# Kernel optimization log

Hardware: AMD Instinct MI355X
Metric: run time of the kernel (lower is better)

Reference implementation:

```python
import jax, jax.numpy as jnp
import numpy as np

N_NODES = 100_000
N_EDGES = 1_600_000
D_IN = 128
D_OUT = 128


def setup_inputs() -> dict:
    key = jax.random.key(0)
    k1, k2, k3, k4, k5 = jax.random.split(key, 5)
    feature = jax.random.normal(k1, (N_NODES, D_IN), dtype=jnp.float32)
    W = jax.random.normal(k2, (D_IN, D_OUT), dtype=jnp.float32) * 0.05
    b = jax.random.normal(k3, (D_OUT,), dtype=jnp.float32) * 0.05
    src = jax.random.randint(k4, (N_EDGES,), 0, N_NODES, dtype=jnp.int32)
    dst = jax.random.randint(k5, (N_EDGES,), 0, N_NODES, dtype=jnp.int32)
    return {"feature": feature, "W": W, "b": b, "src": src, "dst": dst}


def reference(feature, W, b, src, dst):
    N = feature.shape[0]
    # in-degrees (number of incoming edges per node)
    in_deg = jax.ops.segment_sum(
        jnp.ones(dst.shape[0], dtype=feature.dtype), dst, num_segments=N
    )  # [N]
    # degree-constraint scaling: h = x / sqrt(in_deg + 1)
    feat = feature * (1.0 / jnp.sqrt(in_deg + 1.0))[:, None]  # [N, D]
    # copy_u messages + mean reduce over incoming edges
    msg = feat[src]  # [E, D]
    summed = jax.ops.segment_sum(msg, dst, num_segments=N)  # [N, D]
    cnt = in_deg[:, None]
    h = jnp.where(cnt > 0, summed / jnp.maximum(cnt, 1.0), 0.0)  # DGL mean -> 0 for isolated nodes
    # apply_mod linear
    return h @ W + b
```

## Files before the change

### kernel.cpp

```cpp
#include <hip/hip_runtime.h>
#include <math.h>


#define D 128
#define MT 32
#define CAP 48
#define CPAD 16

typedef short short8 __attribute__((ext_vector_type(8)));
typedef float f32x4 __attribute__((ext_vector_type(4)));

__device__ inline unsigned short f2b(float f) {
    unsigned u = __float_as_uint(f);
    return (unsigned short)((u + 0x7FFFu + ((u >> 16) & 1u)) >> 16);
}
#define B2F(u) __uint_as_float(((unsigned)(u)) << 16)

__global__ __launch_bounds__(256) void k_fill(const int* __restrict__ src,
                                              const int* __restrict__ dst,
                                              int* __restrict__ cnt_p,
                                              int* __restrict__ ell,
                                              int ne, int nn) {
    int i = blockIdx.x * 256 + threadIdx.x;
    int e0 = i * 4;
    if (e0 + 4 <= ne) {
        int4 sv = ((const int4*)src)[i];
        int4 dv = ((const int4*)dst)[i];
        int p0 = atomicAdd(&cnt_p[dv.x * CPAD], 1); if (p0 < CAP) ell[(size_t)dv.x * CAP + p0] = sv.x;
        int p1 = atomicAdd(&cnt_p[dv.y * CPAD], 1); if (p1 < CAP) ell[(size_t)dv.y * CAP + p1] = sv.y;
        int p2 = atomicAdd(&cnt_p[dv.z * CPAD], 1); if (p2 < CAP) ell[(size_t)dv.z * CAP + p2] = sv.z;
        int p3 = atomicAdd(&cnt_p[dv.w * CPAD], 1); if (p3 < CAP) ell[(size_t)dv.w * CAP + p3] = sv.w;
    } else {
        for (int e = e0; e < ne; ++e) {
            int d = dst[e];
            int p = atomicAdd(&cnt_p[d * CPAD], 1);
            if (p < CAP) ell[(size_t)d * CAP + p] = src[e];
        }
    }
}

__global__ __launch_bounds__(256) void k_mid(const int* __restrict__ cnt_p,
                                             const float* __restrict__ W,
                                             int* __restrict__ cnt_c,
                                             float* __restrict__ scale,
                                             unsigned short* __restrict__ Wt,
                                             int nn, int sb) {
    int t = threadIdx.x;
    if (blockIdx.x < sb) {
        int n = blockIdx.x * 256 + t;
        if (n < nn) {
            int c = cnt_p[n * CPAD];
            cnt_c[n] = c;
            scale[n] = rsqrtf((float)c + 1.0f);
        }
        return;
    }
    int d = t & 127, k0 = (t >> 7) * 64;
    for (int k = 0; k < 64; ++k)
        Wt[d * D + k0 + k] = f2b(W[(size_t)(k0 + k) * D + d]);
}

__global__ __launch_bounds__(256) void k_gemm(const float* __restrict__ feature,
                                              const unsigned short* __restrict__ Wt,
                                              unsigned short* __restrict__ Yb,
                                              int nn) {
    int t = threadIdx.x;
    int w = t >> 6, l = t & 63;
    int rg = w & 1, ch = w >> 1;
    int base = blockIdx.x * MT;
    int r = base + rg * 16 + (l & 15);
    if (r >= nn) r = nn - 1;
    int kl = (l >> 4) * 8;

    short8 af[4];
    const float* fr = feature + (size_t)r * D;
#pragma unroll
    for (int kc = 0; kc < 4; ++kc) {
        float4 x = *(const float4*)(fr + kc * 32 + kl);
        float4 y = *(const float4*)(fr + kc * 32 + kl + 4);
        short8 a;
        a[0] = (short)f2b(x.x); a[1] = (short)f2b(x.y);
        a[2] = (short)f2b(x.z); a[3] = (short)f2b(x.w);
        a[4] = (short)f2b(y.x); a[5] = (short)f2b(y.y);
        a[6] = (short)f2b(y.z); a[7] = (short)f2b(y.w);
        af[kc] = a;
    }

    f32x4 acc[4];
#pragma unroll
    for (int ct = 0; ct < 4; ++ct) acc[ct] = (f32x4){0.f, 0.f, 0.f, 0.f};

#pragma unroll
    for (int ct = 0; ct < 4; ++ct) {
        int c = ch * 64 + ct * 16 + (l & 15);
        const unsigned short* wr = Wt + (size_t)c * D;
#pragma unroll
        for (int kc = 0; kc < 4; ++kc) {
            short8 b = *(const short8*)(wr + kc * 32 + kl);
            acc[ct] = __builtin_amdgcn_mfma_f32_16x16x32_bf16(af[kc], b, acc[ct], 0, 0, 0);
        }
    }

#pragma unroll
    for (int ct = 0; ct < 4; ++ct) {
        int c = ch * 64 + ct * 16 + (l & 15);
        int r0 = base + rg * 16 + (l >> 4) * 4;
#pragma unroll
        for (int j = 0; j < 4; ++j) {
            int row = r0 + j;
            if (row < nn) Yb[(size_t)row * D + c] = f2b(acc[ct][j]);
        }
    }
}

__global__ __launch_bounds__(256) void k_agg(const unsigned short* __restrict__ Yb,
                                             const float* __restrict__ bias,
                                             const int* __restrict__ cnt,
                                             const float* __restrict__ scale,
                                             const int* __restrict__ ell,
                                             float* __restrict__ out,
                                             int n_nodes) {
    int t = threadIdx.x;
    int wave = t >> 6, lane = t & 63;
    int hw = lane >> 5, sl = lane & 31;
    int base = blockIdx.x * MT;

    const ushort4* y4 = (const ushort4*)Yb;
    float4 bv = ((const float4*)bias)[sl];

#pragma unroll
    for (int j = 0; j < 4; ++j) {
        int n = base + wave * 8 + j * 2 + hw;
        bool valid = (n < n_nodes);
        int c = valid ? cnt[n] : 0;
        if (c > CAP) c = CAP;
        float4 a0 = make_float4(0.f, 0.f, 0.f, 0.f), a1 = a0, a2 = a0, a3 = a0;
        if (c > 0) {
            int slot = sl < c ? sl : c - 1;
            int v = ell[(size_t)n * CAP + slot];
            int iv0 = ((unsigned)v < (unsigned)n_nodes) ? v : 0;
            float sv0 = scale[iv0];
            int eb = 0;
            while (eb < c) {
                int nv = c - eb; if (nv > 32) nv = 32;
                int e = 0;
                for (; e + 8 <= nv; e += 8) {
                    int i0 = __shfl(iv0, e + 0, 32), i1 = __shfl(iv0, e + 1, 32);
                    int i2 = __shfl(iv0, e + 2, 32), i3 = __shfl(iv0, e + 3, 32);
                    int i4 = __shfl(iv0, e + 4, 32), i5 = __shfl(iv0, e + 5, 32);
                    int i6 = __shfl(iv0, e + 6, 32), i7 = __shfl(iv0, e + 7, 32);
                    float c0 = __shfl(sv0, e + 0, 32), c1 = __shfl(sv0, e + 1, 32);
                    float c2 = __shfl(sv0, e + 2, 32), c3 = __shfl(sv0, e + 3, 32);
                    float c4 = __shfl(sv0, e + 4, 32), c5 = __shfl(sv0, e + 5, 32);
                    float c6 = __shfl(sv0, e + 6, 32), c7 = __shfl(sv0, e + 7, 32);
                    ushort4 u0 = y4[(size_t)i0 * 32 + sl], u1 = y4[(size_t)i1 * 32 + sl];
                    ushort4 u2 = y4[(size_t)i2 * 32 + sl], u3 = y4[(size_t)i3 * 32 + sl];
                    ushort4 u4 = y4[(size_t)i4 * 32 + sl], u5 = y4[(size_t)i5 * 32 + sl];
                    ushort4 u6 = y4[(size_t)i6 * 32 + sl], u7 = y4[(size_t)i7 * 32 + sl];
                    a0.x = fmaf(B2F(u0.x), c0, a0.x); a0.y = fmaf(B2F(u0.y), c0, a0.y);
                    a0.z = fmaf(B2F(u0.z), c0, a0.z); a0.w = fmaf(B2F(u0.w), c0, a0.w);
                    a1.x = fmaf(B2F(u1.x), c1, a1.x); a1.y = fmaf(B2F(u1.y), c1, a1.y);
                    a1.z = fmaf(B2F(u1.z), c1, a1.z); a1.w = fmaf(B2F(u1.w), c1, a1.w);
                    a2.x = fmaf(B2F(u2.x), c2, a2.x); a2.y = fmaf(B2F(u2.y), c2, a2.y);
                    a2.z = fmaf(B2F(u2.z), c2, a2.z); a2.w = fmaf(B2F(u2.w), c2, a2.w);
                    a3.x = fmaf(B2F(u3.x), c3, a3.x); a3.y = fmaf(B2F(u3.y), c3, a3.y);
                    a3.z = fmaf(B2F(u3.z), c3, a3.z); a3.w = fmaf(B2F(u3.w), c3, a3.w);
                    a0.x = fmaf(B2F(u4.x), c4, a0.x); a0.y = fmaf(B2F(u4.y), c4, a0.y);
                    a0.z = fmaf(B2F(u4.z), c4, a0.z); a0.w = fmaf(B2F(u4.w), c4, a0.w);
                    a1.x = fmaf(B2F(u5.x), c5, a1.x); a1.y = fmaf(B2F(u5.y), c5, a1.y);
                    a1.z = fmaf(B2F(u5.z), c5, a1.z); a1.w = fmaf(B2F(u5.w), c5, a1.w);
                    a2.x = fmaf(B2F(u6.x), c6, a2.x); a2.y = fmaf(B2F(u6.y), c6, a2.y);
                    a2.z = fmaf(B2F(u6.z), c6, a2.z); a2.w = fmaf(B2F(u6.w), c6, a2.w);
                    a3.x = fmaf(B2F(u7.x), c7, a3.x); a3.y = fmaf(B2F(u7.y), c7, a3.y);
                    a3.z = fmaf(B2F(u7.z), c7, a3.z); a3.w = fmaf(B2F(u7.w), c7, a3.w);
                }
                for (; e + 4 <= nv; e += 4) {
                    int i0 = __shfl(iv0, e + 0, 32), i1 = __shfl(iv0, e + 1, 32);
                    int i2 = __shfl(iv0, e + 2, 32), i3 = __shfl(iv0, e + 3, 32);
                    float c0 = __shfl(sv0, e + 0, 32), c1 = __shfl(sv0, e + 1, 32);
                    float c2 = __shfl(sv0, e + 2, 32), c3 = __shfl(sv0, e + 3, 32);
                    ushort4 u0 = y4[(size_t)i0 * 32 + sl], u1 = y4[(size_t)i1 * 32 + sl];
                    ushort4 u2 = y4[(size_t)i2 * 32 + sl], u3 = y4[(size_t)i3 * 32 + sl];
                    a0.x = fmaf(B2F(u0.x), c0, a0.x); a0.y = fmaf(B2F(u0.y), c0, a0.y);
                    a0.z = fmaf(B2F(u0.z), c0, a0.z); a0.w = fmaf(B2F(u0.w), c0, a0.w);
                    a1.x = fmaf(B2F(u1.x), c1, a1.x); a1.y = fmaf(B2F(u1.y), c1, a1.y);
                    a1.z = fmaf(B2F(u1.z), c1, a1.z); a1.w = fmaf(B2F(u1.w), c1, a1.w);
                    a2.x = fmaf(B2F(u2.x), c2, a2.x); a2.y = fmaf(B2F(u2.y), c2, a2.y);
                    a2.z = fmaf(B2F(u2.z), c2, a2.z); a2.w = fmaf(B2F(u2.w), c2, a2.w);
                    a3.x = fmaf(B2F(u3.x), c3, a3.x); a3.y = fmaf(B2F(u3.y), c3, a3.y);
                    a3.z = fmaf(B2F(u3.z), c3, a3.z); a3.w = fmaf(B2F(u3.w), c3, a3.w);
                }
                for (; e < nv; ++e) {
                    int s = __shfl(iv0, e, 32);
                    float cc = __shfl(sv0, e, 32);
                    ushort4 u = y4[(size_t)s * 32 + sl];
                    a0.x = fmaf(B2F(u.x), cc, a0.x); a0.y = fmaf(B2F(u.y), cc, a0.y);
                    a0.z = fmaf(B2F(u.z), cc, a0.z); a0.w = fmaf(B2F(u.w), cc, a0.w);
                }
                eb += 32;
                if (eb < c) {
                    int rem = c - eb;
                    int slot2 = eb + (sl < rem ? sl : rem - 1);
                    if (slot2 > CAP - 1) slot2 = CAP - 1;
                    int v2 = ell[(size_t)n * CAP + slot2];
                    iv0 = ((unsigned)v2 < (unsigned)n_nodes) ? v2 : 0;
                    sv0 = scale[iv0];
                }
            }
        }
        if (valid) {
            float invn = (c > 0) ? (1.0f / (float)c) : 0.f;
            float4 r;
            r.x = (a0.x + a1.x + a2.x + a3.x) * invn + bv.x;
            r.y = (a0.y + a1.y + a2.y + a3.y) * invn + bv.y;
            r.z = (a0.z + a1.z + a2.z + a3.z) * invn + bv.z;
            r.w = (a0.w + a1.w + a2.w + a3.w) * invn + bv.w;
            ((float4*)out)[(size_t)n * 32 + sl] = r;
        }
    }
}

extern "C" void kernel_launch(void* const* d_in, const int* in_sizes, int n_in,
                              void* d_out, int out_size, void* d_ws, size_t ws_size,
                              hipStream_t stream) {
    const float* feature = (const float*)d_in[0];
    const float* W = (const float*)d_in[1];
    const float* bias = (const float*)d_in[2];
    const int* src = (const int*)d_in[3];
    const int* dst = (const int*)d_in[4];
    float* out = (float*)d_out;

    int n_nodes = in_sizes[0] / D;
    int n_edges = in_sizes[3];
    (void)n_in; (void)out_size; (void)ws_size;

    char* ws = (char*)d_ws;
    size_t o = 0;
    auto alloc = [&](size_t bytes) { void* p = ws + o; o += (bytes + 511) & ~(size_t)511; return p; };
    int* cnt_p = (int*)alloc((size_t)n_nodes * CPAD * 4);
    int* ell = (int*)alloc((size_t)n_nodes * CAP * 4);
    unsigned short* Yb = (unsigned short*)alloc((size_t)n_nodes * D * 2);
    int* cnt_c = (int*)alloc((size_t)n_nodes * 4);
    float* scale = (float*)alloc((size_t)n_nodes * 4);
    unsigned short* Wt = (unsigned short*)alloc((size_t)D * D * 2);

    hipMemsetAsync(cnt_p, 0, (size_t)n_nodes * CPAD * 4, stream);

    int fb = (n_edges + 1023) / 1024;
    int sb = (n_nodes + 255) / 256;
    int tiles = (n_nodes + MT - 1) / MT;

    k_fill<<<fb, 256, 0, stream>>>(src, dst, cnt_p, ell, n_edges, n_nodes);
    k_mid<<<sb + 1, 256, 0, stream>>>(cnt_p, W, cnt_c, scale, Wt, n_nodes, sb);
    k_gemm<<<tiles, 256, 0, stream>>>(feature, Wt, Yb, n_nodes);
    k_agg<<<tiles, 256, 0, stream>>>(Yb, bias, cnt_c, scale, ell, out, n_nodes);
}
```

Before: 339.6 us.

## Store first neighbor indices inline in padded count line with spill array

Uses the otherwise padded 64-byte counter line per node to hold the count plus the first 15 source indices. Extra neighbors go to a separate spill array. The aggregation kernel loads count and up to 31 indices in one pass (16 lanes from the count line, 16 from spill), which removes the separate count array and the dependent count-then-index load chain. Edges past 31 are handled by a scalar per-lane loop, and the inline stores put edge writes on the same cache line as the atomic counter, which may add contention.

```diff
diff --git a/kernel.cpp b/kernel.cpp
--- a/kernel.cpp
+++ b/kernel.cpp
@@ -4,8 +4,10 @@
 
 #define D 128
 #define MT 32
-#define CAP 48
 #define CPAD 16
+#define INL 15
+#define CAPT 48
+#define SCAP 33
 
 typedef short short8 __attribute__((ext_vector_type(8)));
 typedef float f32x4 __attribute__((ext_vector_type(4)));
@@ -18,41 +20,36 @@
 
 __global__ __launch_bounds__(256) void k_fill(const int* __restrict__ src,
                                               const int* __restrict__ dst,
-                                              int* __restrict__ cnt_p,
-                                              int* __restrict__ ell,
+                                              int* __restrict__ cl,
+                                              int* __restrict__ spill,
                                               int ne, int nn) {
+#define PUT(s_, d_) { int p = atomicAdd(&cl[(d_) * CPAD], 1);                  \
+        if (p < INL) cl[(d_) * CPAD + 1 + p] = (s_);                           \
+        else if (p < CAPT) spill[(size_t)(d_) * SCAP + (p - INL)] = (s_); }
     int i = blockIdx.x * 256 + threadIdx.x;
     int e0 = i * 4;
     if (e0 + 4 <= ne) {
         int4 sv = ((const int4*)src)[i];
         int4 dv = ((const int4*)dst)[i];
-        int p0 = atomicAdd(&cnt_p[dv.x * CPAD], 1); if (p0 < CAP) ell[(size_t)dv.x * CAP + p0] = sv.x;
-        int p1 = atomicAdd(&cnt_p[dv.y * CPAD], 1); if (p1 < CAP) ell[(size_t)dv.y * CAP + p1] = sv.y;
-        int p2 = atomicAdd(&cnt_p[dv.z * CPAD], 1); if (p2 < CAP) ell[(size_t)dv.z * CAP + p2] = sv.z;
-        int p3 = atomicAdd(&cnt_p[dv.w * CPAD], 1); if (p3 < CAP) ell[(size_t)dv.w * CAP + p3] = sv.w;
+        PUT(sv.x, dv.x)
+        PUT(sv.y, dv.y)
+        PUT(sv.z, dv.z)
+        PUT(sv.w, dv.w)
     } else {
-        for (int e = e0; e < ne; ++e) {
-            int d = dst[e];
-            int p = atomicAdd(&cnt_p[d * CPAD], 1);
-            if (p < CAP) ell[(size_t)d * CAP + p] = src[e];
-        }
-    }
-}
-
-__global__ __launch_bounds__(256) void k_mid(const int* __restrict__ cnt_p,
+        for (int e = e0; e < ne; ++e) PUT(src[e], dst[e])
+    }
+#undef PUT
+}
+
+__global__ __launch_bounds__(256) void k_mid(const int* __restrict__ cl,
                                              const float* __restrict__ W,
-                                             int* __restrict__ cnt_c,
                                              float* __restrict__ scale,
                                              unsigned short* __restrict__ Wt,
                                              int nn, int sb) {
     int t = threadIdx.x;
     if (blockIdx.x < sb) {
         int n = blockIdx.x * 256 + t;
-        if (n < nn) {
-            int c = cnt_p[n * CPAD];
-            cnt_c[n] = c;
-            scale[n] = rsqrtf((float)c + 1.0f);
-        }
+        if (n < nn) scale[n] = rsqrtf((float)cl[n * CPAD] + 1.0f);
         return;
     }
     int d = t & 127, k0 = (t >> 7) * 64;
@@ -115,9 +112,9 @@
 
 __global__ __launch_bounds__(256) void k_agg(const unsigned short* __restrict__ Yb,
                                              const float* __restrict__ bias,
-                                             const int* __restrict__ cnt,
+                                             const int* __restrict__ cl,
+                                             const int* __restrict__ spill,
                                              const float* __restrict__ scale,
-                                             const int* __restrict__ ell,
                                              float* __restrict__ out,
                                              int n_nodes) {
     int t = threadIdx.x;
@@ -132,80 +129,79 @@
     for (int j = 0; j < 4; ++j) {
         int n = base + wave * 8 + j * 2 + hw;
         bool valid = (n < n_nodes);
-        int c = valid ? cnt[n] : 0;
-        if (c > CAP) c = CAP;
+        int nc = valid ? n : 0;
+        int lv;
+        if (sl < 16) lv = cl[nc * CPAD + sl];
+        else         lv = spill[(size_t)nc * SCAP + (sl - 16)];
+        int c = __shfl(lv, 0, 32);
+        if (!valid) c = 0;
+        if (c > CAPT) c = CAPT;
         float4 a0 = make_float4(0.f, 0.f, 0.f, 0.f), a1 = a0, a2 = a0, a3 = a0;
         if (c > 0) {
-            int slot = sl < c ? sl : c - 1;
-            int v = ell[(size_t)n * CAP + slot];
-            int iv0 = ((unsigned)v < (unsigned)n_nodes) ? v : 0;
+            int iv0 = ((unsigned)lv < (unsigned)n_nodes) ? lv : 0;
             float sv0 = scale[iv0];
-            int eb = 0;
-            while (eb < c) {
-                int nv = c - eb; if (nv > 32) nv = 32;
-                int e = 0;
-                for (; e + 8 <= nv; e += 8) {
-                    int i0 = __shfl(iv0, e + 0, 32), i1 = __shfl(iv0, e + 1, 32);
-                    int i2 = __shfl(iv0, e + 2, 32), i3 = __shfl(iv0, e + 3, 32);
-                    int i4 = __shfl(iv0, e + 4, 32), i5 = __shfl(iv0, e + 5, 32);
-                    int i6 = __shfl(iv0, e + 6, 32), i7 = __shfl(iv0, e + 7, 32);
-                    float c0 = __shfl(sv0, e + 0, 32), c1 = __shfl(sv0, e + 1, 32);
-                    float c2 = __shfl(sv0, e + 2, 32), c3 = __shfl(sv0, e + 3, 32);
-                    float c4 = __shfl(sv0, e + 4, 32), c5 = __shfl(sv0, e + 5, 32);
-                    float c6 = __shfl(sv0, e + 6, 32), c7 = __shfl(sv0, e + 7, 32);
-                    ushort4 u0 = y4[(size_t)i0 * 32 + sl], u1 = y4[(size_t)i1 * 32 + sl];
-                    ushort4 u2 = y4[(size_t)i2 * 32 + sl], u3 = y4[(size_t)i3 * 32 + sl];
-                    ushort4 u4 = y4[(size_t)i4 * 32 + sl], u5 = y4[(size_t)i5 * 32 + sl];
-                    ushort4 u6 = y4[(size_t)i6 * 32 + sl], u7 = y4[(size_t)i7 * 32 + sl];
-                    a0.x = fmaf(B2F(u0.x), c0, a0.x); a0.y = fmaf(B2F(u0.y), c0, a0.y);
-                    a0.z = fmaf(B2F(u0.z), c0, a0.z); a0.w = fmaf(B2F(u0.w), c0, a0.w);
-                    a1.x = fmaf(B2F(u1.x), c1, a1.x); a1.y = fmaf(B2F(u1.y), c1, a1.y);
-                    a1.z = fmaf(B2F(u1.z), c1, a1.z); a1.w = fmaf(B2F(u1.w), c1, a1.w);
-                    a2.x = fmaf(B2F(u2.x), c2, a2.x); a2.y = fmaf(B2F(u2.y), c2, a2.y);
-                    a2.z = fmaf(B2F(u2.z), c2, a2.z); a2.w = fmaf(B2F(u2.w), c2, a2.w);
-                    a3.x = fmaf(B2F(u3.x), c3, a3.x); a3.y = fmaf(B2F(u3.y), c3, a3.y);
-                    a3.z = fmaf(B2F(u3.z), c3, a3.z); a3.w = fmaf(B2F(u3.w), c3, a3.w);
-                    a0.x = fmaf(B2F(u4.x), c4, a0.x); a0.y = fmaf(B2F(u4.y), c4, a0.y);
-                    a0.z = fmaf(B2F(u4.z), c4, a0.z); a0.w = fmaf(B2F(u4.w), c4, a0.w);
-                    a1.x = fmaf(B2F(u5.x), c5, a1.x); a1.y = fmaf(B2F(u5.y), c5, a1.y);
-                    a1.z = fmaf(B2F(u5.z), c5, a1.z); a1.w = fmaf(B2F(u5.w), c5, a1.w);
-                    a2.x = fmaf(B2F(u6.x), c6, a2.x); a2.y = fmaf(B2F(u6.y), c6, a2.y);
-                    a2.z = fmaf(B2F(u6.z), c6, a2.z); a2.w = fmaf(B2F(u6.w), c6, a2.w);
-                    a3.x = fmaf(B2F(u7.x), c7, a3.x); a3.y = fmaf(B2F(u7.y), c7, a3.y);
-                    a3.z = fmaf(B2F(u7.z), c7, a3.z); a3.w = fmaf(B2F(u7.w), c7, a3.w);
-                }
-                for (; e + 4 <= nv; e += 4) {
-                    int i0 = __shfl(iv0, e + 0, 32), i1 = __shfl(iv0, e + 1, 32);
-                    int i2 = __shfl(iv0, e + 2, 32), i3 = __shfl(iv0, e + 3, 32);
-                    float c0 = __shfl(sv0, e + 0, 32), c1 = __shfl(sv0, e + 1, 32);
-                    float c2 = __shfl(sv0, e + 2, 32), c3 = __shfl(sv0, e + 3, 32);
-                    ushort4 u0 = y4[(size_t)i0 * 32 + sl], u1 = y4[(size_t)i1 * 32 + sl];
-                    ushort4 u2 = y4[(size_t)i2 * 32 + sl], u3 = y4[(size_t)i3 * 32 + sl];
-                    a0.x = fmaf(B2F(u0.x), c0, a0.x); a0.y = fmaf(B2F(u0.y), c0, a0.y);
-                    a0.z = fmaf(B2F(u0.z), c0, a0.z); a0.w = fmaf(B2F(u0.w), c0, a0.w);
-                    a1.x = fmaf(B2F(u1.x), c1, a1.x); a1.y = fmaf(B2F(u1.y), c1, a1.y);
-                    a1.z = fmaf(B2F(u1.z), c1, a1.z); a1.w = fmaf(B2F(u1.w), c1, a1.w);
-                    a2.x = fmaf(B2F(u2.x), c2, a2.x); a2.y = fmaf(B2F(u2.y), c2, a2.y);
-                    a2.z = fmaf(B2F(u2.z), c2, a2.z); a2.w = fmaf(B2F(u2.w), c2, a2.w);
-                    a3.x = fmaf(B2F(u3.x), c3, a3.x); a3.y = fmaf(B2F(u3.y), c3, a3.y);
-                    a3.z = fmaf(B2F(u3.z), c3, a3.z); a3.w = fmaf(B2F(u3.w), c3, a3.w);
-                }
-                for (; e < nv; ++e) {
-                    int s = __shfl(iv0, e, 32);
-                    float cc = __shfl(sv0, e, 32);
-                    ushort4 u = y4[(size_t)s * 32 + sl];
-                    a0.x = fmaf(B2F(u.x), cc, a0.x); a0.y = fmaf(B2F(u.y), cc, a0.y);
-                    a0.z = fmaf(B2F(u.z), cc, a0.z); a0.w = fmaf(B2F(u.w), cc, a0.w);
-                }
-                eb += 32;
-                if (eb < c) {
-                    int rem = c - eb;
-                    int slot2 = eb + (sl < rem ? sl : rem - 1);
-                    if (slot2 > CAP - 1) slot2 = CAP - 1;
-                    int v2 = ell[(size_t)n * CAP + slot2];
-                    iv0 = ((unsigned)v2 < (unsigned)n_nodes) ? v2 : 0;
-                    sv0 = scale[iv0];
-                }
+            int nv = c < 31 ? c : 31;
+            int e = 0;
+            for (; e + 8 <= nv; e += 8) {
+                int i0 = __shfl(iv0, e + 1, 32), i1 = __shfl(iv0, e + 2, 32);
+                int i2 = __shfl(iv0, e + 3, 32), i3 = __shfl(iv0, e + 4, 32);
+                int i4 = __shfl(iv0, e + 5, 32), i5 = __shfl(iv0, e + 6, 32);
+                int i6 = __shfl(iv0, e + 7, 32), i7 = __shfl(iv0, e + 8, 32);
+                float c0 = __shfl(sv0, e + 1, 32), c1 = __shfl(sv0, e + 2, 32);
+                float c2 = __shfl(sv0, e + 3, 32), c3 = __shfl(sv0, e + 4, 32);
+                float c4 = __shfl(sv0, e + 5, 32), c5 = __shfl(sv0, e + 6, 32);
+                float c6 = __shfl(sv0, e + 7, 32), c7 = __shfl(sv0, e + 8, 32);
+                ushort4 u0 = y4[(size_t)i0 * 32 + sl], u1 = y4[(size_t)i1 * 32 + sl];
+                ushort4 u2 = y4[(size_t)i2 * 32 + sl], u3 = y4[(size_t)i3 * 32 + sl];
+                ushort4 u4 = y4[(size_t)i4 * 32 + sl], u5 = y4[(size_t)i5 * 32 + sl];
+                ushort4 u6 = y4[(size_t)i6 * 32 + sl], u7 = y4[(size_t)i7 * 32 + sl];
+                a0.x = fmaf(B2F(u0.x), c0, a0.x); a0.y = fmaf(B2F(u0.y), c0, a0.y);
+                a0.z = fmaf(B2F(u0.z), c0, a0.z); a0.w = fmaf(B2F(u0.w), c0, a0.w);
+                a1.x = fmaf(B2F(u1.x), c1, a1.x); a1.y = fmaf(B2F(u1.y), c1, a1.y);
+                a1.z = fmaf(B2F(u1.z), c1, a1.z); a1.w = fmaf(B2F(u1.w), c1, a1.w);
+                a2.x = fmaf(B2F(u2.x), c2, a2.x); a2.y = fmaf(B2F(u2.y), c2, a2.y);
+                a2.z = fmaf(B2F(u2.z), c2, a2.z); a2.w = fmaf(B2F(u2.w), c2, a2.w);
+                a3.x = fmaf(B2F(u3.x), c3, a3.x); a3.y = fmaf(B2F(u3.y), c3, a3.y);
+                a3.z = fmaf(B2F(u3.z), c3, a3.z); a3.w = fmaf(B2F(u3.w), c3, a3.w);
+                a0.x = fmaf(B2F(u4.x), c4, a0.x); a0.y = fmaf(B2F(u4.y), c4, a0.y);
+                a0.z = fmaf(B2F(u4.z), c4, a0.z); a0.w = fmaf(B2F(u4.w), c4, a0.w);
+                a1.x = fmaf(B2F(u5.x), c5, a1.x); a1.y = fmaf(B2F(u5.y), c5, a1.y);
+                a1.z = fmaf(B2F(u5.z), c5, a1.z); a1.w = fmaf(B2F(u5.w), c5, a1.w);
+                a2.x = fmaf(B2F(u6.x), c6, a2.x); a2.y = fmaf(B2F(u6.y), c6, a2.y);
+                a2.z = fmaf(B2F(u6.z), c6, a2.z); a2.w = fmaf(B2F(u6.w), c6, a2.w);
+                a3.x = fmaf(B2F(u7.x), c7, a3.x); a3.y = fmaf(B2F(u7.y), c7, a3.y);
+                a3.z = fmaf(B2F(u7.z), c7, a3.z); a3.w = fmaf(B2F(u7.w), c7, a3.w);
+            }
+            for (; e + 4 <= nv; e += 4) {
+                int i0 = __shfl(iv0, e + 1, 32), i1 = __shfl(iv0, e + 2, 32);
+                int i2 = __shfl(iv0, e + 3, 32), i3 = __shfl(iv0, e + 4, 32);
+                float c0 = __shfl(sv0, e + 1, 32), c1 = __shfl(sv0, e + 2, 32);
+                float c2 = __shfl(sv0, e + 3, 32), c3 = __shfl(sv0, e + 4, 32);
+                ushort4 u0 = y4[(size_t)i0 * 32 + sl], u1 = y4[(size_t)i1 * 32 + sl];
+                ushort4 u2 = y4[(size_t)i2 * 32 + sl], u3 = y4[(size_t)i3 * 32 + sl];
+                a0.x = fmaf(B2F(u0.x), c0, a0.x); a0.y = fmaf(B2F(u0.y), c0, a0.y);
+                a0.z = fmaf(B2F(u0.z), c0, a0.z); a0.w = fmaf(B2F(u0.w), c0, a0.w);
+                a1.x = fmaf(B2F(u1.x), c1, a1.x); a1.y = fmaf(B2F(u1.y), c1, a1.y);
+                a1.z = fmaf(B2F(u1.z), c1, a1.z); a1.w = fmaf(B2F(u1.w), c1, a1.w);
+                a2.x = fmaf(B2F(u2.x), c2, a2.x); a2.y = fmaf(B2F(u2.y), c2, a2.y);
+                a2.z = fmaf(B2F(u2.z), c2, a2.z); a2.w = fmaf(B2F(u2.w), c2, a2.w);
+                a3.x = fmaf(B2F(u3.x), c3, a3.x); a3.y = fmaf(B2F(u3.y), c3, a3.y);
+                a3.z = fmaf(B2F(u3.z), c3, a3.z); a3.w = fmaf(B2F(u3.w), c3, a3.w);
+            }
+            for (; e < nv; ++e) {
+                int s = __shfl(iv0, e + 1, 32);
+                float cc = __shfl(sv0, e + 1, 32);
+                ushort4 u = y4[(size_t)s * 32 + sl];
+                a0.x = fmaf(B2F(u.x), cc, a0.x); a0.y = fmaf(B2F(u.y), cc, a0.y);
+                a0.z = fmaf(B2F(u.z), cc, a0.z); a0.w = fmaf(B2F(u.w), cc, a0.w);
+            }
+            for (int p = 31; p < c; ++p) {
+                int s = spill[(size_t)nc * SCAP + (p - INL)];
+                s = ((unsigned)s < (unsigned)n_nodes) ? s : 0;
+                float cc = scale[s];
+                ushort4 u = y4[(size_t)s * 32 + sl];
+                a0.x = fmaf(B2F(u.x), cc, a0.x); a0.y = fmaf(B2F(u.y), cc, a0.y);
+                a0.z = fmaf(B2F(u.z), cc, a0.z); a0.w = fmaf(B2F(u.w), cc, a0.w);
             }
         }
         if (valid) {
@@ -237,21 +233,20 @@
     char* ws = (char*)d_ws;
     size_t o = 0;
     auto alloc = [&](size_t bytes) { void* p = ws + o; o += (bytes + 511) & ~(size_t)511; return p; };
-    int* cnt_p = (int*)alloc((size_t)n_nodes * CPAD * 4);
-    int* ell = (int*)alloc((size_t)n_nodes * CAP * 4);
+    int* cl = (int*)alloc((size_t)n_nodes * CPAD * 4);
+    int* spill = (int*)alloc((size_t)n_nodes * SCAP * 4);
     unsigned short* Yb = (unsigned short*)alloc((size_t)n_nodes * D * 2);
-    int* cnt_c = (int*)alloc((size_t)n_nodes * 4);
     float* scale = (float*)alloc((size_t)n_nodes * 4);
     unsigned short* Wt = (unsigned short*)alloc((size_t)D * D * 2);
 
-    hipMemsetAsync(cnt_p, 0, (size_t)n_nodes * CPAD * 4, stream);
+    hipMemsetAsync(cl, 0, (size_t)n_nodes * CPAD * 4, stream);
 
     int fb = (n_edges + 1023) / 1024;
     int sb = (n_nodes + 255) / 256;
     int tiles = (n_nodes + MT - 1) / MT;
 
-    k_fill<<<fb, 256, 0, stream>>>(src, dst, cnt_p, ell, n_edges, n_nodes);
-    k_mid<<<sb + 1, 256, 0, stream>>>(cnt_p, W, cnt_c, scale, Wt, n_nodes, sb);
+    k_fill<<<fb, 256, 0, stream>>>(src, dst, cl, spill, n_edges, n_nodes);
+    k_mid<<<sb + 1, 256, 0, stream>>>(cl, W, scale, Wt, n_nodes, sb);
     k_gemm<<<tiles, 256, 0, stream>>>(feature, Wt, Yb, n_nodes);
-    k_agg<<<tiles, 256, 0, stream>>>(Yb, bias, cnt_c, scale, ell, out, n_nodes);
-}
+    k_agg<<<tiles, 256, 0, stream>>>(Yb, bias, cl, spill, scale, out, n_nodes);
+}
```

Result: faster. 291.0 us (-14.3%).
